# Performance work log

Measured on AMD Instinct MI355X. Metric: run time of the kernel, lower is better.

Reference implementation:

```python
import jax, jax.numpy as jnp
import numpy as np

N = 50000      # nodes
E = 600000     # edges
D = 128        # embedding_dimension
R = 2          # num_relations
DESC = 768; TW = 768; NUMF = 5; CATF = 3
EPS = 1e-5


def setup_inputs() -> dict:
    key = jax.random.key(0)
    ks = jax.random.split(key, 32)
    f32 = jnp.float32

    def rn(k, shape):
        return jax.random.normal(k, shape, dtype=f32)

    def w(k, fan_in, shape):
        return jax.random.normal(k, shape, dtype=f32) * (1.0 / np.sqrt(fan_in))

    inp = {}
    inp["desc_embedding"] = rn(ks[0], (N, DESC))
    inp["tweet_embedding"] = rn(ks[1], (N, TW))
    inp["num_feature"] = rn(ks[2], (N, NUMF))
    inp["cat_feature"] = rn(ks[3], (N, CATF))
    inp["edge_index"] = jax.random.randint(ks[4], (2, E), 0, N, dtype=jnp.int32)
    inp["edge_type"] = jax.random.randint(ks[5], (E,), 0, R, dtype=jnp.int32)
    q = D // 4
    inp["Wd"] = w(ks[6], DESC, (DESC, q)); inp["bd"] = jnp.zeros((q,), f32)
    inp["Wt"] = w(ks[7], TW, (TW, q));     inp["bt"] = jnp.zeros((q,), f32)
    inp["Wn"] = w(ks[8], NUMF, (NUMF, q)); inp["bn"] = jnp.zeros((q,), f32)
    inp["Wc"] = w(ks[9], CATF, (CATF, q)); inp["bc"] = jnp.zeros((q,), f32)
    inp["W1"] = w(ks[10], D, (D, D)); inp["b1"] = jnp.zeros((D,), f32)
    inp["rg1_w"] = w(ks[11], D, (R, D, D)); inp["rg1_root"] = w(ks[12], D, (D, D)); inp["rg1_bias"] = jnp.zeros((D,), f32)
    inp["ln1_g"] = jnp.ones((D,), f32); inp["ln1_b"] = jnp.zeros((D,), f32)
    inp["rg2_w"] = w(ks[13], D, (R, D, D)); inp["rg2_root"] = w(ks[14], D, (D, D)); inp["rg2_bias"] = jnp.zeros((D,), f32)
    inp["ln2_g"] = jnp.ones((D,), f32); inp["ln2_b"] = jnp.zeros((D,), f32)
    inp["W2"] = w(ks[15], D, (D, D)); inp["b2"] = jnp.zeros((D,), f32)
    inp["W3"] = w(ks[16], D, (D, 1)); inp["b3"] = jnp.zeros((1,), f32)
    return inp


def _leaky(x):
    return jnp.where(x > 0, x, 0.01 * x)


def _rgcn_max(x, edge_index, edge_type, rel_w, root_w, bias):
    # PyG RGCNConv(aggr='max'): out = x @ root + bias + sum_r (max-agg of x_j over rel-r edges) @ W_r
    src, dst = edge_index[0], edge_index[1]
    xs = x[src]  # [E, D] gathered source features
    out = x @ root_w + bias
    for r in range(R):
        msg = jnp.where((edge_type == r)[:, None], xs, -jnp.inf)
        agg = jax.ops.segment_max(msg, dst, num_segments=N)  # [N, D]
        agg = jnp.where(jnp.isinf(agg), 0.0, agg)            # empty slots -> 0
        out = out + agg @ rel_w[r]
    return out


def _graph_layernorm(x, gamma, beta):
    # torch_geometric.nn.LayerNorm, mode='graph': normalize over ALL nodes+channels of the graph
    mu = jnp.mean(x)
    xc = x - mu
    var = jnp.mean(xc * xc)
    return xc / jnp.sqrt(var + EPS) * gamma + beta


def reference(desc_embedding, tweet_embedding, num_feature, cat_feature,
              edge_index, edge_type,
              Wd, bd, Wt, bt, Wn, bn, Wc, bc,
              W1, b1, rg1_w, rg1_root, rg1_bias, ln1_g, ln1_b,
              rg2_w, rg2_root, rg2_bias, ln2_g, ln2_b,
              W2, b2, W3, b3):
    x = jnp.concatenate([
        _leaky(desc_embedding @ Wd + bd),
        _leaky(tweet_embedding @ Wt + bt),
        _leaky(num_feature @ Wn + bn),
        _leaky(cat_feature @ Wc + bc),
    ], axis=1)                                   # [N, D]
    x = _leaky(x @ W1 + b1)
    x = _rgcn_max(x, edge_index, edge_type, rg1_w, rg1_root, rg1_bias)
    x = _graph_layernorm(x, ln1_g, ln1_b)
    # dropout: eval mode (identity)
    x = _rgcn_max(x, edge_index, edge_type, rg2_w, rg2_root, rg2_bias)
    x = _graph_layernorm(x, ln2_g, ln2_b)
    x = _leaky(x @ W2 + b2)
    x = jax.nn.sigmoid(x @ W3 + b3)
    return x.reshape(-1)                          # [N]
```

## Files before the change

kernel.cpp:

```cpp
#include <hip/hip_runtime.h>
#include <cstdint>
#include <cstddef>

#define NN 50000
#define EE 600000
#define DD 128
#define NSEG (NN*2)
#define NPART ((NSEG + 255) / 256)

typedef short bf16x8 __attribute__((ext_vector_type(8)));
typedef float f32x4 __attribute__((ext_vector_type(4)));

__device__ __forceinline__ float leaky_f(float x){ return x > 0.f ? x : 0.01f*x; }

__device__ __forceinline__ unsigned short f2bf(float f){
    unsigned u = __float_as_uint(f);
    u += 0x7fffu + ((u >> 16) & 1u);
    return (unsigned short)(u >> 16);
}

__device__ __forceinline__ void split8(const float* a, bf16x8& hi, bf16x8& lo){
#pragma unroll
    for (int j=0;j<8;j++){
        unsigned u  = __float_as_uint(a[j]);
        unsigned uh = u & 0xFFFF0000u;
        hi[j] = (short)(uh >> 16);
        float lf = a[j] - __uint_as_float(uh);
        lo[j] = (short)(__float_as_uint(lf) >> 16);
    }
}

__global__ __launch_bounds__(256) void proj_k(
    const float* __restrict__ A0, const float* __restrict__ A1,
    const float* __restrict__ B0, const float* __restrict__ B1,
    const float* __restrict__ bias0, const float* __restrict__ bias1,
    float* __restrict__ C, int M)
{
    constexpr int K = 768, BN = 32, CT = 2;
    __shared__ unsigned short sB[4*BN*40];
    const int tid = threadIdx.x;
    const int lane = tid & 63;
    const int wv = tid >> 6;
    const int q = lane >> 4, n16 = lane & 15;
    const int bm = blockIdx.x * 64;
    const int arow = bm + wv*16 + n16;
    const float* A = blockIdx.y ? A1 : A0;
    const float* B = blockIdx.y ? B1 : B0;
    const float* bias = blockIdx.y ? bias1 : bias0;
    const int c0 = blockIdx.y * 32;

    f32x4 acc[CT];
#pragma unroll
    for (int c=0;c<CT;c++) acc[c] = (f32x4){0.f,0.f,0.f,0.f};

    for (int kb=0; kb<K/128; kb++) {
        __syncthreads();
        {
            const int n = tid % BN;
            const int kq0 = tid / BN;
#pragma unroll
            for (int kq = kq0; kq < 32; kq += 8) {
                const float* gp = B + (size_t)(kb*128 + kq*4)*BN + n;
                float v0 = gp[0], v1 = gp[BN], v2 = gp[2*BN], v3 = gp[3*BN];
                int ks = kq >> 3, kk = (kq & 7)*4;
                int sa = (ks*BN + n)*40 + kk;
                *reinterpret_cast<unsigned*>(&sB[sa])   = (unsigned)f2bf(v0) | ((unsigned)f2bf(v1) << 16);
                *reinterpret_cast<unsigned*>(&sB[sa+2]) = (unsigned)f2bf(v2) | ((unsigned)f2bf(v3) << 16);
            }
        }
        __syncthreads();
#pragma unroll
        for (int ks=0; ks<4; ks++) {
            float a[8];
            if (arow < M) {
                const float* ap = A + (size_t)arow*K + kb*128 + ks*32 + q*8;
                float4 t0 = *reinterpret_cast<const float4*>(ap);
                float4 t1 = *reinterpret_cast<const float4*>(ap+4);
                a[0]=t0.x;a[1]=t0.y;a[2]=t0.z;a[3]=t0.w;
                a[4]=t1.x;a[5]=t1.y;a[6]=t1.z;a[7]=t1.w;
            } else {
#pragma unroll
                for (int j=0;j<8;j++) a[j]=0.f;
            }
            bf16x8 ah, al;
            split8(a, ah, al);
#pragma unroll
            for (int c=0;c<CT;c++) {
                bf16x8 b = *reinterpret_cast<const bf16x8*>(&sB[(ks*BN + c*16 + n16)*40 + q*8]);
                acc[c] = __builtin_amdgcn_mfma_f32_16x16x32_bf16(ah, b, acc[c], 0,0,0);
                acc[c] = __builtin_amdgcn_mfma_f32_16x16x32_bf16(al, b, acc[c], 0,0,0);
            }
        }
    }
    const int orow = bm + wv*16 + q*4;
#pragma unroll
    for (int c=0;c<CT;c++) {
        float bb = bias[c*16 + n16];
#pragma unroll
        for (int i=0;i<4;i++) {
            int r = orow + i;
            if (r < M) C[(size_t)r*DD + c0 + c*16 + n16] = leaky_f(acc[c][i] + bb);
        }
    }
}

template<int S,int BFMASK,int LEAKY,int HEAD,int LNRED>
__global__ __launch_bounds__(256) void mfgemm_k(
    const void* __restrict__ A0, const void* __restrict__ A1, const void* __restrict__ A2,
    const float* __restrict__ B0, const float* __restrict__ B1, const float* __restrict__ B2,
    const float* __restrict__ bias, float* __restrict__ C, int M,
    const float* __restrict__ W3, const float* __restrict__ b3,
    float* __restrict__ red, float* __restrict__ outv)
{
    constexpr int BN = 128, CT = 8;
    __shared__ unsigned short sB[4*BN*40];
    const int tid = threadIdx.x;
    const int lane = tid & 63;
    const int wv = tid >> 6;
    const int q = lane >> 4, n16 = lane & 15;
    const int bm = blockIdx.x * 64;
    const int arow = bm + wv*16 + n16;

    f32x4 acc[CT];
#pragma unroll
    for (int c=0;c<CT;c++) acc[c] = (f32x4){0.f,0.f,0.f,0.f};

    const void* As[3] = {A0, A1, A2};
    const float* Bs[3] = {B0, B1, B2};

#pragma unroll
    for (int s=0; s<S; s++) {
        const bool f32s = !((BFMASK >> s) & 1);
        __syncthreads();
        {
            const float* Bp = Bs[s];
            const int n = tid % BN;
            const int kq0 = tid / BN;
#pragma unroll
            for (int kq = kq0; kq < 32; kq += 2) {
                const float* gp = Bp + (size_t)(kq*4)*BN + n;
                float v0 = gp[0], v1 = gp[BN], v2 = gp[2*BN], v3 = gp[3*BN];
                int ks = kq >> 3, kk = (kq & 7)*4;
                int sa = (ks*BN + n)*40 + kk;
                *reinterpret_cast<unsigned*>(&sB[sa])   = (unsigned)f2bf(v0) | ((unsigned)f2bf(v1) << 16);
                *reinterpret_cast<unsigned*>(&sB[sa+2]) = (unsigned)f2bf(v2) | ((unsigned)f2bf(v3) << 16);
            }
        }
        __syncthreads();
#pragma unroll
        for (int ks=0; ks<4; ks++) {
            bf16x8 ah, al;
            if (f32s) {
                float a[8];
                if (arow < M) {
                    const float* ap = (const float*)As[s] + (size_t)arow*DD + ks*32 + q*8;
                    float4 t0 = *reinterpret_cast<const float4*>(ap);
                    float4 t1 = *reinterpret_cast<const float4*>(ap+4);
                    a[0]=t0.x;a[1]=t0.y;a[2]=t0.z;a[3]=t0.w;
                    a[4]=t1.x;a[5]=t1.y;a[6]=t1.z;a[7]=t1.w;
                } else {
#pragma unroll
                    for (int j=0;j<8;j++) a[j]=0.f;
                }
                split8(a, ah, al);
            } else {
                if (arow < M) {
                    const unsigned short* ap = (const unsigned short*)As[s]
                        + (size_t)arow*DD + ks*32 + q*8;
                    ah = *reinterpret_cast<const bf16x8*>(ap);
                } else {
#pragma unroll
                    for (int j=0;j<8;j++) ah[j]=0;
                }
            }
#pragma unroll
            for (int c=0;c<CT;c++) {
                bf16x8 b = *reinterpret_cast<const bf16x8*>(&sB[(ks*BN + c*16 + n16)*40 + q*8]);
                acc[c] = __builtin_amdgcn_mfma_f32_16x16x32_bf16(ah, b, acc[c], 0,0,0);
                if (f32s)
                    acc[c] = __builtin_amdgcn_mfma_f32_16x16x32_bf16(al, b, acc[c], 0,0,0);
            }
        }
    }

    const int orow = bm + wv*16 + q*4;
    if (HEAD) {
        float w3c[CT];
#pragma unroll
        for (int c=0;c<CT;c++) w3c[c] = W3[c*16 + n16];
        float bb3 = b3[0];
#pragma unroll
        for (int i=0;i<4;i++) {
            float t = 0.f;
#pragma unroll
            for (int c=0;c<CT;c++) {
                float v = acc[c][i] + bias[c*16 + n16];
                if (LEAKY) v = leaky_f(v);
                t = fmaf(v, w3c[c], t);
            }
#pragma unroll
            for (int m=1;m<16;m<<=1) t += __shfl_xor(t, m);
            int r = orow + i;
            if (n16 == 0 && r < M) outv[r] = 1.f / (1.f + expf(-(t + bb3)));
        }
    } else {
        float s = 0.f, ss = 0.f;
#pragma unroll
        for (int c=0;c<CT;c++) {
            float bb = bias[c*16 + n16];
#pragma unroll
            for (int i=0;i<4;i++) {
                int r = orow + i;
                if (r < M) {
                    float v = acc[c][i] + bb;
                    if (LEAKY) v = leaky_f(v);
                    C[(size_t)r*DD + c*16 + n16] = v;
                    if (LNRED) { s += v; ss = fmaf(v, v, ss); }
                }
            }
        }
        if (LNRED) {
#pragma unroll
            for (int o=32;o>0;o>>=1) { s += __shfl_down(s,o); ss += __shfl_down(ss,o); }
            __shared__ float rs[4], rss[4];
            if (lane == 0) { rs[wv] = s; rss[wv] = ss; }
            __syncthreads();
            if (tid == 0) {
                atomicAdd(&red[0], rs[0]+rs[1]+rs[2]+rs[3]);
                atomicAdd(&red[1], rss[0]+rss[1]+rss[2]+rss[3]);
            }
        }
    }
}

__global__ void numcat_k(const float* __restrict__ numf, const float* __restrict__ catf,
                         const float* __restrict__ Wn, const float* __restrict__ bn,
                         const float* __restrict__ Wc, const float* __restrict__ bc,
                         float* __restrict__ x)
{
    int t = blockIdx.x*blockDim.x + threadIdx.x;
    if (t >= NN*64) return;
    int n = t >> 6, c = t & 63;
    if (c < 32) {
        float acc = bn[c];
#pragma unroll
        for (int k=0;k<5;k++) acc = fmaf(numf[n*5+k], Wn[k*32+c], acc);
        x[(size_t)n*DD + 64 + c] = leaky_f(acc);
    } else {
        int cc = c - 32;
        float acc = bc[cc];
#pragma unroll
        for (int k=0;k<3;k++) acc = fmaf(catf[n*3+k], Wc[k*32+cc], acc);
        x[(size_t)n*DD + 96 + cc] = leaky_f(acc);
    }
}

__global__ void zero_int_k(int* __restrict__ p, int n)
{
    int i = blockIdx.x*blockDim.x + threadIdx.x;
    if (i < n) p[i] = 0;
}

__global__ void hist_k(const int* __restrict__ ei, const int* __restrict__ et,
                       int* __restrict__ deg)
{
    int e = blockIdx.x*blockDim.x + threadIdx.x;
    if (e >= EE) return;
    atomicAdd(&deg[ei[EE + e]*2 + et[e]], 1);
}

__global__ __launch_bounds__(256) void part_reduce_k(const int* __restrict__ deg,
                                                     int* __restrict__ part)
{
    __shared__ int s[256];
    int t = threadIdx.x;
    int i = blockIdx.x*256 + t;
    s[t] = (i < NSEG) ? deg[i] : 0;
    __syncthreads();
#pragma unroll
    for (int o=128;o>0;o>>=1) {
        if (t < o) s[t] += s[t+o];
        __syncthreads();
    }
    if (t == 0) part[blockIdx.x] = s[0];
}

__global__ __launch_bounds__(512) void part_scan_k(int* __restrict__ part)
{
    __shared__ int ps[512];
    int t = threadIdx.x;
    int v = (t < NPART) ? part[t] : 0;
    ps[t] = v; __syncthreads();
    for (int o=1;o<512;o<<=1) {
        int u = (t >= o) ? ps[t-o] : 0;
        __syncthreads();
        ps[t] += u;
        __syncthreads();
    }
    if (t < NPART) part[t] = ps[t] - v;
}

__global__ __launch_bounds__(256) void final_scan_k(const int* __restrict__ deg,
                                                    const int* __restrict__ part,
                                                    int* __restrict__ offs,
                                                    int* __restrict__ cursor)
{
    __shared__ int ps[256];
    int t = threadIdx.x;
    int i = blockIdx.x*256 + t;
    int d = (i < NSEG) ? deg[i] : 0;
    ps[t] = d; __syncthreads();
    for (int o=1;o<256;o<<=1) {
        int u = (t >= o) ? ps[t-o] : 0;
        __syncthreads();
        ps[t] += u;
        __syncthreads();
    }
    if (i < NSEG) {
        int off = part[blockIdx.x] + ps[t] - d;
        offs[i] = off; cursor[i] = off;
    }
    if (blockIdx.x == 0 && t == 0) offs[NSEG] = EE;
}

__global__ void place_k(const int* __restrict__ ei, const int* __restrict__ et,
                        int* __restrict__ cursor, unsigned short* __restrict__ csr)
{
    int e = blockIdx.x*blockDim.x + threadIdx.x;
    if (e >= EE) return;
    int r = et[e], dst = ei[EE + e], src = ei[e];
    int pos = atomicAdd(&cursor[dst*2 + r], 1);
    csr[pos] = (unsigned short)src;
}

__global__ void gather2_k(const float* __restrict__ x, const int* __restrict__ offs,
                          const unsigned short* __restrict__ csr,
                          unsigned short* __restrict__ aggb, float* __restrict__ red)
{
    if (blockIdx.x == 0 && threadIdx.x < 4) red[threadIdx.x] = 0.f;
    int seg = (blockIdx.x*blockDim.x + threadIdx.x) >> 6;
    int lane = threadIdx.x & 63;
    if (seg >= NSEG) return;
    int node = seg >> 1, r = seg & 1;
    int beg = offs[seg], end = offs[seg+1];
    float2 m = make_float2(-3.402823466e+38f, -3.402823466e+38f);
    for (int j=beg;j<end;j++) {
        int src = csr[j];
        float2 v = *reinterpret_cast<const float2*>(x + (size_t)src*DD + lane*2);
        m.x = fmaxf(m.x, v.x);
        m.y = fmaxf(m.y, v.y);
    }
    if (beg == end) { m.x = 0.f; m.y = 0.f; }
    unsigned o = (unsigned)f2bf(m.x) | ((unsigned)f2bf(m.y) << 16);
    *reinterpret_cast<unsigned*>(aggb + (size_t)r*NN*DD + (size_t)node*DD + lane*2) = o;
}

__global__ void norm_k(float* __restrict__ x, const float* __restrict__ g,
                       const float* __restrict__ b, const float* __restrict__ red)
{
    const float inv = 1.f / (float)(NN*DD);
    float mu  = red[0] * inv;
    float var = red[1] * inv - mu*mu;
    float rstd = rsqrtf(var + 1e-5f);
    int i = blockIdx.x*blockDim.x + threadIdx.x;
    int c = i & 127;
    x[i] = (x[i]-mu)*rstd*g[c] + b[c];
}

extern "C" void kernel_launch(void* const* d_in, const int* in_sizes, int n_in,
                              void* d_out, int out_size, void* d_ws, size_t ws_size,
                              hipStream_t stream)
{
    const float* desc  = (const float*)d_in[0];
    const float* tweet = (const float*)d_in[1];
    const float* numf  = (const float*)d_in[2];
    const float* catf  = (const float*)d_in[3];
    const int*   ei    = (const int*)d_in[4];
    const int*   et    = (const int*)d_in[5];
    const float* Wd=(const float*)d_in[6];  const float* bd=(const float*)d_in[7];
    const float* Wt=(const float*)d_in[8];  const float* bt=(const float*)d_in[9];
    const float* Wn=(const float*)d_in[10]; const float* bn=(const float*)d_in[11];
    const float* Wc=(const float*)d_in[12]; const float* bc=(const float*)d_in[13];
    const float* W1=(const float*)d_in[14]; const float* b1=(const float*)d_in[15];
    const float* rg1w=(const float*)d_in[16]; const float* rg1root=(const float*)d_in[17];
    const float* rg1b=(const float*)d_in[18];
    const float* ln1g=(const float*)d_in[19]; const float* ln1b=(const float*)d_in[20];
    const float* rg2w=(const float*)d_in[21]; const float* rg2root=(const float*)d_in[22];
    const float* rg2b=(const float*)d_in[23];
    const float* ln2g=(const float*)d_in[24]; const float* ln2b=(const float*)d_in[25];
    const float* W2=(const float*)d_in[26]; const float* b2=(const float*)d_in[27];
    const float* W3=(const float*)d_in[28]; const float* b3=(const float*)d_in[29];
    float* out = (float*)d_out;

    float* xa  = (float*)d_ws;
    float* xb  = xa + (size_t)NN*DD;
    unsigned short* aggb = (unsigned short*)(xb + (size_t)NN*DD);
    unsigned short* aggb0 = aggb;
    unsigned short* aggb1 = aggb + (size_t)NN*DD;
    float* red = (float*)(aggb + (size_t)2*NN*DD);
    int*   deg    = (int*)(red + 4);
    int*   offs   = deg + NSEG;
    int*   cursor = offs + NSEG + 1;
    int*   part   = cursor + NSEG;
    unsigned short* csr = (unsigned short*)(part + NPART);

    dim3 blk(256);
    const int mblocks = (NN + 63) / 64;
    const int nelm_blocks = (NN*DD)/256;
    const int edge_blocks = (EE+255)/256;
    const int seg_blocks  = (NSEG*64)/256;

    proj_k<<<dim3(mblocks,2), blk, 0, stream>>>(desc, tweet, Wd, Wt, bd, bt, xa, NN);
    numcat_k<<<(NN*64)/256, 256, 0, stream>>>(numf, catf, Wn, bn, Wc, bc, xa);

    zero_int_k<<<(NSEG+255)/256, 256, 0, stream>>>(deg, NSEG);
    hist_k<<<edge_blocks, 256, 0, stream>>>(ei, et, deg);
    part_reduce_k<<<NPART, 256, 0, stream>>>(deg, part);
    part_scan_k<<<1, 512, 0, stream>>>(part);
    final_scan_k<<<NPART, 256, 0, stream>>>(deg, part, offs, cursor);
    place_k<<<edge_blocks, 256, 0, stream>>>(ei, et, cursor, csr);

    hipLaunchKernelGGL((mfgemm_k<1,0,1,0,0>), dim3(mblocks), blk, 0, stream,
                       xa, nullptr, nullptr, W1, nullptr, nullptr, b1, xb, NN,
                       nullptr, nullptr, nullptr, nullptr);

    gather2_k<<<seg_blocks, 256, 0, stream>>>(xb, offs, csr, aggb, red);
    hipLaunchKernelGGL((mfgemm_k<3,6,0,0,1>), dim3(mblocks), blk, 0, stream,
                       xb, aggb0, aggb1,
                       rg1root, rg1w, rg1w + (size_t)DD*DD, rg1b, xa, NN,
                       nullptr, nullptr, red, nullptr);
    norm_k<<<nelm_blocks, 256, 0, stream>>>(xa, ln1g, ln1b, red);

    gather2_k<<<seg_blocks, 256, 0, stream>>>(xa, offs, csr, aggb, red);
    hipLaunchKernelGGL((mfgemm_k<3,6,0,0,1>), dim3(mblocks), blk, 0, stream,
                       xa, aggb0, aggb1,
                       rg2root, rg2w, rg2w + (size_t)DD*DD, rg2b, xb, NN,
                       nullptr, nullptr, red, nullptr);
    norm_k<<<nelm_blocks, 256, 0, stream>>>(xb, ln2g, ln2b, red);

    hipLaunchKernelGGL((mfgemm_k<1,0,1,1,0>), dim3(mblocks), blk, 0, stream,
                       xb, nullptr, nullptr, W2, nullptr, nullptr, b2, nullptr, NN,
                       W3, b3, nullptr, out);
}
```

Baseline: 818.7 us.

## Prepack GEMM weights into bf16 MFMA fragment layout and prefetch A in registers

Two new kernels convert all the dense weights into bf16, pre-arranged in per-lane MFMA fragment order in workspace. The projection and GEMM kernels then load B fragments straight from global memory instead of converting and staging them through LDS with __syncthreads. The A-operand loads are double-buffered in registers so the next k-slice is fetched while the current one runs on MFMA. This adds two small launches per call, raises register pressure, and reuses the degree buffer as storage for the packed weights.

```diff
diff --git a/kernel.cpp b/kernel.cpp
--- a/kernel.cpp
+++ b/kernel.cpp
@@ -30,14 +30,54 @@
     }
 }
 
+
+__global__ __launch_bounds__(256) void pack768_k(
+    const float* __restrict__ Wd, const float* __restrict__ Wt,
+    unsigned short* __restrict__ out)
+{
+    int idx = blockIdx.x*256 + threadIdx.x;
+    int m = idx / 24576;
+    int r = idx - m*24576;
+    int kb   = r >> 12;
+    int ks   = (r >> 10) & 3;
+    int c    = (r >> 9) & 1;
+    int lane = (r >> 3) & 63;
+    int j    = r & 7;
+    int q = lane >> 4, n16 = lane & 15;
+    int k = kb*128 + ks*32 + q*8 + j;
+    int n = c*16 + n16;
+    const float* W = m ? Wt : Wd;
+    out[idx] = f2bf(W[k*32 + n]);
+}
+
+__global__ __launch_bounds__(256) void pack128_k(
+    const float* __restrict__ W0, const float* __restrict__ W1,
+    const float* __restrict__ W2, const float* __restrict__ W3,
+    const float* __restrict__ W4, const float* __restrict__ W5,
+    const float* __restrict__ W6, const float* __restrict__ W7,
+    unsigned short* __restrict__ out)
+{
+    int idx = blockIdx.x*256 + threadIdx.x;
+    int m = idx >> 14;
+    int r = idx & 16383;
+    int ks   = r >> 12;
+    int c    = (r >> 9) & 7;
+    int lane = (r >> 3) & 63;
+    int j    = r & 7;
+    int q = lane >> 4, n16 = lane & 15;
+    int k = ks*32 + q*8 + j;
+    int n = c*16 + n16;
+    const float* Ws[8] = {W0,W1,W2,W3,W4,W5,W6,W7};
+    out[idx] = f2bf(Ws[m][k*128 + n]);
+}
+
 __global__ __launch_bounds__(256) void proj_k(
     const float* __restrict__ A0, const float* __restrict__ A1,
-    const float* __restrict__ B0, const float* __restrict__ B1,
+    const unsigned short* __restrict__ Bp,
     const float* __restrict__ bias0, const float* __restrict__ bias1,
     float* __restrict__ C, int M)
 {
-    constexpr int K = 768, BN = 32, CT = 2;
-    __shared__ unsigned short sB[4*BN*40];
+    constexpr int K = 768, CT = 2;
     const int tid = threadIdx.x;
     const int lane = tid & 63;
     const int wv = tid >> 6;
@@ -45,53 +85,57 @@
     const int bm = blockIdx.x * 64;
     const int arow = bm + wv*16 + n16;
     const float* A = blockIdx.y ? A1 : A0;
-    const float* B = blockIdx.y ? B1 : B0;
+    const unsigned short* bp = Bp + (size_t)blockIdx.y * 24576 + lane*8;
     const float* bias = blockIdx.y ? bias1 : bias0;
     const int c0 = blockIdx.y * 32;
+    const bool rowok = arow < M;
+    const float* arowp = A + (size_t)(rowok ? arow : 0) * K;
 
     f32x4 acc[CT];
 #pragma unroll
     for (int c=0;c<CT;c++) acc[c] = (f32x4){0.f,0.f,0.f,0.f};
 
-    for (int kb=0; kb<K/128; kb++) {
-        __syncthreads();
-        {
-            const int n = tid % BN;
-            const int kq0 = tid / BN;
-#pragma unroll
-            for (int kq = kq0; kq < 32; kq += 8) {
-                const float* gp = B + (size_t)(kb*128 + kq*4)*BN + n;
-                float v0 = gp[0], v1 = gp[BN], v2 = gp[2*BN], v3 = gp[3*BN];
-                int ks = kq >> 3, kk = (kq & 7)*4;
-                int sa = (ks*BN + n)*40 + kk;
-                *reinterpret_cast<unsigned*>(&sB[sa])   = (unsigned)f2bf(v0) | ((unsigned)f2bf(v1) << 16);
-                *reinterpret_cast<unsigned*>(&sB[sa+2]) = (unsigned)f2bf(v2) | ((unsigned)f2bf(v3) << 16);
-            }
-        }
-        __syncthreads();
-#pragma unroll
-        for (int ks=0; ks<4; ks++) {
-            float a[8];
-            if (arow < M) {
-                const float* ap = A + (size_t)arow*K + kb*128 + ks*32 + q*8;
-                float4 t0 = *reinterpret_cast<const float4*>(ap);
-                float4 t1 = *reinterpret_cast<const float4*>(ap+4);
-                a[0]=t0.x;a[1]=t0.y;a[2]=t0.z;a[3]=t0.w;
-                a[4]=t1.x;a[5]=t1.y;a[6]=t1.z;a[7]=t1.w;
-            } else {
-#pragma unroll
-                for (int j=0;j<8;j++) a[j]=0.f;
-            }
-            bf16x8 ah, al;
-            split8(a, ah, al);
-#pragma unroll
-            for (int c=0;c<CT;c++) {
-                bf16x8 b = *reinterpret_cast<const bf16x8*>(&sB[(ks*BN + c*16 + n16)*40 + q*8]);
-                acc[c] = __builtin_amdgcn_mfma_f32_16x16x32_bf16(ah, b, acc[c], 0,0,0);
-                acc[c] = __builtin_amdgcn_mfma_f32_16x16x32_bf16(al, b, acc[c], 0,0,0);
-            }
-        }
-    }
+    float4 ar[2][8];
+
+#define PROJ_LOADA(BUF, KB) { \
+    _Pragma("unroll") \
+    for (int ks=0; ks<4; ks++){ \
+        const float* ap = arowp + (KB)*128 + ks*32 + q*8; \
+        if (rowok){ \
+            ar[BUF][ks*2]   = *reinterpret_cast<const float4*>(ap); \
+            ar[BUF][ks*2+1] = *reinterpret_cast<const float4*>(ap+4); \
+        } else { \
+            ar[BUF][ks*2]   = make_float4(0.f,0.f,0.f,0.f); \
+            ar[BUF][ks*2+1] = make_float4(0.f,0.f,0.f,0.f); \
+        } \
+    } }
+
+#define PROJ_COMP(BUF, KB) { \
+    bf16x8 br[8]; \
+    _Pragma("unroll") \
+    for (int f=0; f<8; f++) \
+        br[f] = *reinterpret_cast<const bf16x8*>(bp + (size_t)((KB)*8 + f)*512); \
+    _Pragma("unroll") \
+    for (int ks=0; ks<4; ks++){ \
+        float a[8]; \
+        float4 t0 = ar[BUF][ks*2], t1 = ar[BUF][ks*2+1]; \
+        a[0]=t0.x;a[1]=t0.y;a[2]=t0.z;a[3]=t0.w; \
+        a[4]=t1.x;a[5]=t1.y;a[6]=t1.z;a[7]=t1.w; \
+        bf16x8 ah, al; split8(a, ah, al); \
+        _Pragma("unroll") \
+        for (int c=0;c<CT;c++){ \
+            acc[c] = __builtin_amdgcn_mfma_f32_16x16x32_bf16(ah, br[ks*2+c], acc[c], 0,0,0); \
+            acc[c] = __builtin_amdgcn_mfma_f32_16x16x32_bf16(al, br[ks*2+c], acc[c], 0,0,0); \
+        } \
+    } }
+
+    PROJ_LOADA(0, 0)
+#pragma unroll
+    for (int kb=0; kb<6; kb++){
+        if (kb < 5) { PROJ_LOADA(((kb+1)&1), (kb+1)) }
+        PROJ_COMP((kb&1), kb)
+    }
+
     const int orow = bm + wv*16 + q*4;
 #pragma unroll
     for (int c=0;c<CT;c++) {
@@ -102,86 +146,88 @@
             if (r < M) C[(size_t)r*DD + c0 + c*16 + n16] = leaky_f(acc[c][i] + bb);
         }
     }
-}
-
-template<int S,int BFMASK,int LEAKY,int HEAD,int LNRED>
+#undef PROJ_LOADA
+#undef PROJ_COMP
+}
+
+template<int S,int BFMASK,int LEAKY,int HEAD,int LNRED,int BI0,int BI1,int BI2>
 __global__ __launch_bounds__(256) void mfgemm_k(
     const void* __restrict__ A0, const void* __restrict__ A1, const void* __restrict__ A2,
-    const float* __restrict__ B0, const float* __restrict__ B1, const float* __restrict__ B2,
+    const unsigned short* __restrict__ Bp,
     const float* __restrict__ bias, float* __restrict__ C, int M,
     const float* __restrict__ W3, const float* __restrict__ b3,
     float* __restrict__ red, float* __restrict__ outv)
 {
-    constexpr int BN = 128, CT = 8;
-    __shared__ unsigned short sB[4*BN*40];
+    constexpr int CT = 8;
     const int tid = threadIdx.x;
     const int lane = tid & 63;
     const int wv = tid >> 6;
     const int q = lane >> 4, n16 = lane & 15;
     const int bm = blockIdx.x * 64;
     const int arow = bm + wv*16 + n16;
+    const bool rowok = arow < M;
 
     f32x4 acc[CT];
 #pragma unroll
     for (int c=0;c<CT;c++) acc[c] = (f32x4){0.f,0.f,0.f,0.f};
 
     const void* As[3] = {A0, A1, A2};
-    const float* Bs[3] = {B0, B1, B2};
-
-#pragma unroll
-    for (int s=0; s<S; s++) {
-        const bool f32s = !((BFMASK >> s) & 1);
-        __syncthreads();
-        {
-            const float* Bp = Bs[s];
-            const int n = tid % BN;
-            const int kq0 = tid / BN;
-#pragma unroll
-            for (int kq = kq0; kq < 32; kq += 2) {
-                const float* gp = Bp + (size_t)(kq*4)*BN + n;
-                float v0 = gp[0], v1 = gp[BN], v2 = gp[2*BN], v3 = gp[3*BN];
-                int ks = kq >> 3, kk = (kq & 7)*4;
-                int sa = (ks*BN + n)*40 + kk;
-                *reinterpret_cast<unsigned*>(&sB[sa])   = (unsigned)f2bf(v0) | ((unsigned)f2bf(v1) << 16);
-                *reinterpret_cast<unsigned*>(&sB[sa+2]) = (unsigned)f2bf(v2) | ((unsigned)f2bf(v3) << 16);
-            }
-        }
-        __syncthreads();
-#pragma unroll
-        for (int ks=0; ks<4; ks++) {
-            bf16x8 ah, al;
-            if (f32s) {
-                float a[8];
-                if (arow < M) {
-                    const float* ap = (const float*)As[s] + (size_t)arow*DD + ks*32 + q*8;
-                    float4 t0 = *reinterpret_cast<const float4*>(ap);
-                    float4 t1 = *reinterpret_cast<const float4*>(ap+4);
-                    a[0]=t0.x;a[1]=t0.y;a[2]=t0.z;a[3]=t0.w;
-                    a[4]=t1.x;a[5]=t1.y;a[6]=t1.z;a[7]=t1.w;
-                } else {
-#pragma unroll
-                    for (int j=0;j<8;j++) a[j]=0.f;
-                }
-                split8(a, ah, al);
-            } else {
-                if (arow < M) {
-                    const unsigned short* ap = (const unsigned short*)As[s]
-                        + (size_t)arow*DD + ks*32 + q*8;
-                    ah = *reinterpret_cast<const bf16x8*>(ap);
-                } else {
-#pragma unroll
-                    for (int j=0;j<8;j++) ah[j]=0;
-                }
-            }
-#pragma unroll
-            for (int c=0;c<CT;c++) {
-                bf16x8 b = *reinterpret_cast<const bf16x8*>(&sB[(ks*BN + c*16 + n16)*40 + q*8]);
-                acc[c] = __builtin_amdgcn_mfma_f32_16x16x32_bf16(ah, b, acc[c], 0,0,0);
-                if (f32s)
-                    acc[c] = __builtin_amdgcn_mfma_f32_16x16x32_bf16(al, b, acc[c], 0,0,0);
-            }
-        }
-    }
+    constexpr int BI[3] = {BI0, BI1, BI2};
+    const unsigned short* bpl = Bp + lane*8;
+
+    float4 arf[2][2];
+    bf16x8 arb[2];
+
+#define MG_LOADA(BUF, SS, KS) { \
+    if (!((BFMASK >> (SS)) & 1)) { \
+        if (rowok){ \
+            const float* ap = (const float*)As[SS] + (size_t)arow*DD + (KS)*32 + q*8; \
+            arf[BUF][0] = *reinterpret_cast<const float4*>(ap); \
+            arf[BUF][1] = *reinterpret_cast<const float4*>(ap+4); \
+        } else { \
+            arf[BUF][0] = make_float4(0.f,0.f,0.f,0.f); \
+            arf[BUF][1] = make_float4(0.f,0.f,0.f,0.f); \
+        } \
+    } else { \
+        if (rowok){ \
+            const unsigned short* ap = (const unsigned short*)As[SS] + (size_t)arow*DD + (KS)*32 + q*8; \
+            arb[BUF] = *reinterpret_cast<const bf16x8*>(ap); \
+        } else { \
+            _Pragma("unroll") for (int jj=0;jj<8;jj++) arb[BUF][jj]=0; \
+        } \
+    } }
+
+#define MG_COMP(BUF, SS, KS) { \
+    bf16x8 br[8]; \
+    const unsigned short* bpp = bpl + BI[SS]*16384 + (KS)*4096; \
+    _Pragma("unroll") \
+    for (int c=0;c<8;c++) br[c] = *reinterpret_cast<const bf16x8*>(bpp + c*512); \
+    if (!((BFMASK >> (SS)) & 1)) { \
+        float a[8]; \
+        float4 t0 = arf[BUF][0], t1 = arf[BUF][1]; \
+        a[0]=t0.x;a[1]=t0.y;a[2]=t0.z;a[3]=t0.w; \
+        a[4]=t1.x;a[5]=t1.y;a[6]=t1.z;a[7]=t1.w; \
+        bf16x8 ah, al; split8(a, ah, al); \
+        _Pragma("unroll") \
+        for (int c=0;c<CT;c++){ \
+            acc[c] = __builtin_amdgcn_mfma_f32_16x16x32_bf16(ah, br[c], acc[c], 0,0,0); \
+            acc[c] = __builtin_amdgcn_mfma_f32_16x16x32_bf16(al, br[c], acc[c], 0,0,0); \
+        } \
+    } else { \
+        _Pragma("unroll") \
+        for (int c=0;c<CT;c++) \
+            acc[c] = __builtin_amdgcn_mfma_f32_16x16x32_bf16(arb[BUF], br[c], acc[c], 0,0,0); \
+    } }
+
+    MG_LOADA(0, 0, 0)
+#pragma unroll
+    for (int t=0; t<S*4; t++){
+        const int nt = t+1;
+        if (nt < S*4) { MG_LOADA((nt&1), (nt>>2), (nt&3)) }
+        MG_COMP((t&1), (t>>2), (t&3))
+    }
+#undef MG_LOADA
+#undef MG_COMP
 
     const int orow = bm + wv*16 + q*4;
     if (HEAD) {
@@ -404,14 +450,14 @@
     int*   part   = cursor + NSEG;
     unsigned short* csr = (unsigned short*)(part + NPART);
 
+    unsigned short* bp768 = (unsigned short*)deg;
+    unsigned short* bp128 = bp768 + 49152;
+
     dim3 blk(256);
     const int mblocks = (NN + 63) / 64;
     const int nelm_blocks = (NN*DD)/256;
     const int edge_blocks = (EE+255)/256;
     const int seg_blocks  = (NSEG*64)/256;
-
-    proj_k<<<dim3(mblocks,2), blk, 0, stream>>>(desc, tweet, Wd, Wt, bd, bt, xa, NN);
-    numcat_k<<<(NN*64)/256, 256, 0, stream>>>(numf, catf, Wn, bn, Wc, bc, xa);
 
     zero_int_k<<<(NSEG+255)/256, 256, 0, stream>>>(deg, NSEG);
     hist_k<<<edge_blocks, 256, 0, stream>>>(ei, et, deg);
@@ -420,25 +466,30 @@
     final_scan_k<<<NPART, 256, 0, stream>>>(deg, part, offs, cursor);
     place_k<<<edge_blocks, 256, 0, stream>>>(ei, et, cursor, csr);
 
-    hipLaunchKernelGGL((mfgemm_k<1,0,1,0,0>), dim3(mblocks), blk, 0, stream,
-                       xa, nullptr, nullptr, W1, nullptr, nullptr, b1, xb, NN,
+    pack768_k<<<192, 256, 0, stream>>>(Wd, Wt, bp768);
+    pack128_k<<<512, 256, 0, stream>>>(W1, rg1root, rg1w, rg1w + (size_t)DD*DD,
+                                       rg2root, rg2w, rg2w + (size_t)DD*DD, W2, bp128);
+
+    proj_k<<<dim3(mblocks,2), blk, 0, stream>>>(desc, tweet, bp768, bd, bt, xa, NN);
+    numcat_k<<<(NN*64)/256, 256, 0, stream>>>(numf, catf, Wn, bn, Wc, bc, xa);
+
+    hipLaunchKernelGGL((mfgemm_k<1,0,1,0,0,0,0,0>), dim3(mblocks), blk, 0, stream,
+                       xa, nullptr, nullptr, bp128, b1, xb, NN,
                        nullptr, nullptr, nullptr, nullptr);
 
     gather2_k<<<seg_blocks, 256, 0, stream>>>(xb, offs, csr, aggb, red);
-    hipLaunchKernelGGL((mfgemm_k<3,6,0,0,1>), dim3(mblocks), blk, 0, stream,
-                       xb, aggb0, aggb1,
-                       rg1root, rg1w, rg1w + (size_t)DD*DD, rg1b, xa, NN,
+    hipLaunchKernelGGL((mfgemm_k<3,6,0,0,1,1,2,3>), dim3(mblocks), blk, 0, stream,
+                       xb, aggb0, aggb1, bp128, rg1b, xa, NN,
                        nullptr, nullptr, red, nullptr);
     norm_k<<<nelm_blocks, 256, 0, stream>>>(xa, ln1g, ln1b, red);
 
     gather2_k<<<seg_blocks, 256, 0, stream>>>(xa, offs, csr, aggb, red);
-    hipLaunchKernelGGL((mfgemm_k<3,6,0,0,1>), dim3(mblocks), blk, 0, stream,
-                       xa, aggb0, aggb1,
-                       rg2root, rg2w, rg2w + (size_t)DD*DD, rg2b, xb, NN,
+    hipLaunchKernelGGL((mfgemm_k<3,6,0,0,1,4,5,6>), dim3(mblocks), blk, 0, stream,
+                       xa, aggb0, aggb1, bp128, rg2b, xb, NN,
                        nullptr, nullptr, red, nullptr);
     norm_k<<<nelm_blocks, 256, 0, stream>>>(xb, ln2g, ln2b, red);
 
-    hipLaunchKernelGGL((mfgemm_k<1,0,1,1,0>), dim3(mblocks), blk, 0, stream,
-                       xb, nullptr, nullptr, W2, nullptr, nullptr, b2, nullptr, NN,
+    hipLaunchKernelGGL((mfgemm_k<1,0,1,1,0,7,0,0>), dim3(mblocks), blk, 0, stream,
+                       xb, nullptr, nullptr, bp128, b2, nullptr, NN,
                        W3, b3, nullptr, out);
 }
```

After: 765.3 us. 1.07x faster.
